# Kernel tuning notes

Measured on AMD Instinct MI355X. Metric: run time of the kernel, lower is better.

Reference implementation:

```python
import jax, jax.numpy as jnp
import numpy as np

HEAD_SIZE = 64
N_EMBED = 1024

def setup_inputs() -> dict:
    key = jax.random.key(0)
    kx, kk, kq, kv = jax.random.split(key, 4)
    x = jax.random.normal(kx, (8, 2048, N_EMBED), dtype=jnp.float32)
    # torch nn.Linear weights: [out_features, in_features]
    s = 1.0 / np.sqrt(N_EMBED)
    Wk = jax.random.uniform(kk, (HEAD_SIZE, N_EMBED), jnp.float32, -s, s)
    Wq = jax.random.uniform(kq, (HEAD_SIZE, N_EMBED), jnp.float32, -s, s)
    Wv = jax.random.uniform(kv, (HEAD_SIZE, N_EMBED), jnp.float32, -s, s)
    return {"x": x, "Wk": Wk, "Wq": Wq, "Wv": Wv}

def reference(x, Wk, Wq, Wv):
    B, T, C = x.shape
    k = x @ Wk.T  # [B,T,H]
    q = x @ Wq.T
    v = x @ Wv.T
    # NOTE: original computes k @ q^T and scales by sqrt(C)=sqrt(n_embed)
    wei = jnp.einsum('btd,bsd->bts', k, q) / jnp.sqrt(jnp.float32(C))
    mask = jnp.tril(jnp.ones((T, T), dtype=bool))
    wei = jnp.where(mask, wei, -jnp.inf)
    wei = jax.nn.softmax(wei, axis=-1)
    return wei @ v  # [B,T,H]
```

## Files before the change

kernel.cpp:

```cpp
#include <hip/hip_runtime.h>
#include <hip/hip_bf16.h>


typedef __attribute__((ext_vector_type(8))) short short8;
typedef __attribute__((ext_vector_type(4))) float f32x4;
typedef __attribute__((ext_vector_type(16))) float f32x16;
typedef unsigned int u32;

#define BATCH 8
#define T 2048
#define CDIM 1024
#define HD 64
#define QK_SCALE 0.04508422f

static __device__ __forceinline__ short f2bf(float f) {
    return __builtin_bit_cast(short, __float2bfloat16(f));
}
static __device__ __forceinline__ float bf2f(unsigned short s) {
    u32 u = ((u32)s) << 16;
    return __builtin_bit_cast(float, u);
}
static __device__ __forceinline__ u32 packbf(float lo, float hi) {
    return (u32)(unsigned short)f2bf(lo) | ((u32)(unsigned short)f2bf(hi) << 16);
}
static __device__ __forceinline__ f32x4 mfma16(short8 a, short8 b, f32x4 c) {
    return __builtin_amdgcn_mfma_f32_16x16x32_bf16(a, b, c, 0, 0, 0);
}
static __device__ __forceinline__ f32x16 mfma32(short8 a, short8 b, f32x16 c) {
    return __builtin_amdgcn_mfma_f32_32x32x16_bf16(a, b, c, 0, 0, 0);
}

__global__ __launch_bounds__(256) void wcvt_kernel(
    const float* __restrict__ Wk, const float* __restrict__ Wq,
    const float* __restrict__ Wv, short* __restrict__ wfrag)
{
    const int t = blockIdx.x * 256 + threadIdx.x;
    const int lane = t & 63, kk = (t >> 6) & 31, d16 = (t >> 11) & 3, p = t >> 13;
    const float* __restrict__ W = (p == 0) ? Wk : (p == 1 ? Wq : Wv);
    const float sc = (p == 0) ? QK_SCALE : 1.0f;
    const float* src = W + (size_t)(d16 * 16 + (lane & 15)) * CDIM
                         + kk * 32 + ((lane >> 4) & 3) * 8;
    f32x4 a = *(const f32x4*)src;
    f32x4 b = *(const f32x4*)(src + 4);
    short8 o;
#pragma unroll
    for (int e = 0; e < 4; ++e) { o[e] = f2bf(a[e] * sc); o[e + 4] = f2bf(b[e] * sc); }
    *(short8*)(wfrag + (size_t)t * 8) = o;
}

#define XLOAD(KC) { \
    xr0 = *(const f32x4*)(xsrc + (KC) * 64); \
    xr1 = *(const f32x4*)(xsrc + (KC) * 64 + 4); }

#define XWRITE(BASE) { \
    short8 v = { f2bf(xr0[0]), f2bf(xr0[1]), f2bf(xr0[2]), f2bf(xr0[3]), \
                 f2bf(xr1[0]), f2bf(xr1[1]), f2bf(xr1[2]), f2bf(xr1[3]) }; \
    *(short8*)((BASE) + srow * 128 + ((sseg * 16) ^ ((srow & 7) << 4))) = v; }

#define BLOAD(DST, KC) \
    _Pragma("unroll") for (int u = 0; u < 6; ++u) \
        DST[u] = *(const short8*)&wfrag[(size_t)((cg * 3 + (u % 3)) * 32 + (KC) * 2 + (u / 3)) * 512 + lane * 8];

#define COMPUTE(XBASE, B) \
    _Pragma("unroll") for (int kkL = 0; kkL < 2; ++kkL) { \
        short8 af0 = *(short8*)((XBASE) + c * 128 + ((kkL * 64 + g * 16) ^ ((c & 7) << 4))); \
        short8 af1 = *(short8*)((XBASE) + (16 + c) * 128 + ((kkL * 64 + g * 16) ^ ((c & 7) << 4))); \
        _Pragma("unroll") for (int j = 0; j < 3; ++j) { \
            acc[0][j] = mfma16(af0, B[kkL * 3 + j], acc[0][j]); \
            acc[1][j] = mfma16(af1, B[kkL * 3 + j], acc[1][j]); } }

__global__ __launch_bounds__(256) void proj_kernel(
    const float* __restrict__ x, const short* __restrict__ wfrag,
    short* __restrict__ kfrag, short* __restrict__ qfrag, short* __restrict__ vfrag)
{
    __shared__ __align__(16) char lds[16384];
    char* X0 = lds;
    char* X1 = lds + 4096;

    const int tid = threadIdx.x, cg = tid >> 6, lane = tid & 63;
    const int c = lane & 15, g = lane >> 4;
    const int srow = tid >> 3, sseg = tid & 7;
    const int row0 = blockIdx.x * 32;
    const float* __restrict__ xsrc = x + (size_t)(row0 + srow) * CDIM + sseg * 8;

    f32x4 acc[2][3] = {};
    short8 bA[6], bB[6];
    f32x4 xr0, xr1;

    XLOAD(0)
    XWRITE(X0)
    BLOAD(bA, 0)
    __syncthreads();

    for (int c2 = 0; c2 < 8; ++c2) {
        const int cB = 2 * c2 + 1;
        BLOAD(bB, cB)
        XLOAD(cB)
        COMPUTE(X0, bA)
        XWRITE(X1)
        __syncthreads();
        if (c2 < 7) {
            BLOAD(bA, cB + 1)
            XLOAD(cB + 1)
        }
        COMPUTE(X1, bB)
        if (c2 < 7) {
            XWRITE(X0)
        }
        __syncthreads();
    }

    short* st_k = (short*)lds;
    short* st_q = (short*)(lds + 4608);
    short* st_v = (short*)(lds + 9216);
#pragma unroll
    for (int j = 0; j < 3; ++j) {
        const int q = cg * 3 + j, p = q >> 2, d16 = q & 3;
#pragma unroll
        for (int rh = 0; rh < 2; ++rh)
#pragma unroll
            for (int r = 0; r < 4; ++r) {
                const int mrow = rh * 16 + g * 4 + r;
                const short v = f2bf(acc[rh][j][r]);
                if (p == 0)      st_k[mrow * 72 + d16 * 16 + c] = v;
                else if (p == 1) st_q[mrow * 72 + d16 * 16 + c] = v;
                else             st_v[(d16 * 16 + c) * 40 + mrow] = v;
            }
    }
    __syncthreads();

    const int b = row0 >> 11, i = (row0 & 2047) >> 5;
    const size_t tb = ((size_t)(b * 64 + i)) * 4;
    const int l5 = lane & 31, h = lane >> 5;
    const int fq = cg;

    short8 kv = *(short8*)&st_k[l5 * 72 + fq * 16 + h * 8];
    *(short8*)&kfrag[(tb + fq) * 512 + lane * 8] = kv;
    short8 qv = *(short8*)&st_q[l5 * 72 + fq * 16 + h * 8];
    *(short8*)&qfrag[(tb + fq) * 512 + lane * 8] = qv;
    const int dh = fq >> 1, ssub = fq & 1;
    short8 vv = *(short8*)&st_v[(dh * 32 + l5) * 40 + ssub * 16 + h * 8];
    *(short8*)&vfrag[(tb + fq) * 512 + lane * 8] = vv;
}

__global__ __launch_bounds__(512) void attn_kernel(
    const short* __restrict__ kfrag, const short* __restrict__ qfrag,
    const short* __restrict__ vfrag, float* __restrict__ out)
{
    const int tid = threadIdx.x, wid = tid >> 6, lane = tid & 63;
    const int l5 = lane & 31, h = lane >> 5;
    const int bx = blockIdx.x;
    const int i = 63 - (bx >> 3);
    const int b = bx & 7;
    const int t0 = i * 32;

    __shared__ u32   sO[8][32][32];
    __shared__ float sML[8][2][32];

    const short* __restrict__ kb = kfrag + ((size_t)(b * 64 + i)) * 2048;
    const short* __restrict__ qb = qfrag + ((size_t)b * 64) * 2048;
    const short* __restrict__ vb = vfrag + ((size_t)b * 64) * 2048;

    short8 kf[4];
#pragma unroll
    for (int ks = 0; ks < 4; ++ks)
        kf[ks] = *(const short8*)&kb[ks * 512 + lane * 8];

    float m = -1e30f, l = 0.f;
    f32x16 o0 = {}, o1 = {};

    short8 qf[4], vf[4], qn[4], vn[4];
#pragma unroll
    for (int ks = 0; ks < 4; ++ks) {
        qf[ks] = *(const short8*)&qb[((size_t)wid * 4 + ks) * 512 + lane * 8];
        vf[ks] = *(const short8*)&vb[((size_t)wid * 4 + ks) * 512 + lane * 8];
    }

    for (int st = wid; st <= i; st += 8) {
        f32x16 Cs = {};
#pragma unroll
        for (int ks = 0; ks < 4; ++ks)
            Cs = mfma32(qf[ks], kf[ks], Cs);

        if (st + 8 <= i) {
#pragma unroll
            for (int ks = 0; ks < 4; ++ks) {
                qn[ks] = *(const short8*)&qb[((size_t)(st + 8) * 4 + ks) * 512 + lane * 8];
                vn[ks] = *(const short8*)&vb[((size_t)(st + 8) * 4 + ks) * 512 + lane * 8];
            }
        }

        if (st == i) {
#pragma unroll
            for (int r = 0; r < 16; ++r) {
                const int srow = (r & 3) + 8 * (r >> 2) + 4 * h;
                if (srow > l5) Cs[r] = -1e30f;
            }
        }
        float mx = fmaxf(Cs[0], Cs[1]);
#pragma unroll
        for (int r = 2; r < 16; ++r) mx = fmaxf(mx, Cs[r]);
        mx = fmaxf(mx, __shfl_xor(mx, 32));
        if (!__all(mx <= m)) {
            const float mnew = fmaxf(m, mx);
            const float alpha = exp2f(m - mnew);
            m = mnew;
            l *= alpha;
#pragma unroll
            for (int r = 0; r < 16; ++r) { o0[r] *= alpha; o1[r] *= alpha; }
        }
        u32 pk[8];
        float rs = 0.f;
#pragma unroll
        for (int q = 0; q < 8; ++q) {
            const float e0 = exp2f(Cs[2 * q] - m);
            const float e1 = exp2f(Cs[2 * q + 1] - m);
            rs += e0 + e1;
            pk[q] = packbf(e0, e1);
        }
        rs += __shfl_xor(rs, 32);
        l += rs;

        u32 w0 = pk[0], w2 = pk[2];
        asm volatile("v_permlane32_swap_b32 %0, %1" : "+v"(w0), "+v"(w2));
        u32 w1 = pk[1], w3 = pk[3];
        asm volatile("v_permlane32_swap_b32 %0, %1" : "+v"(w1), "+v"(w3));
        u32 w4 = pk[4], w6 = pk[6];
        asm volatile("v_permlane32_swap_b32 %0, %1" : "+v"(w4), "+v"(w6));
        u32 w5 = pk[5], w7 = pk[7];
        asm volatile("v_permlane32_swap_b32 %0, %1" : "+v"(w5), "+v"(w7));
        short8 pf0, pf1;
        pf0[0] = (short)(w0 & 0xffff); pf0[1] = (short)(w0 >> 16);
        pf0[2] = (short)(w1 & 0xffff); pf0[3] = (short)(w1 >> 16);
        pf0[4] = (short)(w2 & 0xffff); pf0[5] = (short)(w2 >> 16);
        pf0[6] = (short)(w3 & 0xffff); pf0[7] = (short)(w3 >> 16);
        pf1[0] = (short)(w4 & 0xffff); pf1[1] = (short)(w4 >> 16);
        pf1[2] = (short)(w5 & 0xffff); pf1[3] = (short)(w5 >> 16);
        pf1[4] = (short)(w6 & 0xffff); pf1[5] = (short)(w6 >> 16);
        pf1[6] = (short)(w7 & 0xffff); pf1[7] = (short)(w7 >> 16);

        o0 = mfma32(vf[0], pf0, o0);
        o0 = mfma32(vf[1], pf1, o0);
        o1 = mfma32(vf[2], pf0, o1);
        o1 = mfma32(vf[3], pf1, o1);

#pragma unroll
        for (int ks = 0; ks < 4; ++ks) { qf[ks] = qn[ks]; vf[ks] = vn[ks]; }
    }

#pragma unroll
    for (int q = 0; q < 8; ++q) {
        const int dp = (q & 1) + 4 * (q >> 1) + 2 * h;
        sO[wid][dp][l5]      = packbf(o0[2 * q], o0[2 * q + 1]);
        sO[wid][16 + dp][l5] = packbf(o1[2 * q], o1[2 * q + 1]);
    }
    if (h == 0) { sML[wid][0][l5] = m; sML[wid][1][l5] = l; }
    __syncthreads();

    float M = -1e30f;
#pragma unroll
    for (int p = 0; p < 8; ++p) M = fmaxf(M, sML[p][0][l5]);
    float L = 0.f;
    float av[4] = {};
#pragma unroll
    for (int p = 0; p < 8; ++p) {
        const float w = exp2f(sML[p][0][l5] - M);
        L += w * sML[p][1][l5];
#pragma unroll
        for (int dd2 = 0; dd2 < 2; ++dd2) {
            const u32 v = sO[p][wid * 4 + h * 2 + dd2][l5];
            av[2 * dd2]     += w * bf2f((unsigned short)(v & 0xffff));
            av[2 * dd2 + 1] += w * bf2f((unsigned short)(v >> 16));
        }
    }
    const float inv = 1.f / L;
    f32x4 r = { av[0] * inv, av[1] * inv, av[2] * inv, av[3] * inv };
    *(f32x4*)&out[((size_t)b * T + t0 + l5) * HD + wid * 8 + h * 4] = r;
}

extern "C" void kernel_launch(void* const* d_in, const int* in_sizes, int n_in,
                              void* d_out, int out_size, void* d_ws, size_t ws_size,
                              hipStream_t stream) {
    const float* x  = (const float*)d_in[0];
    const float* Wk = (const float*)d_in[1];
    const float* Wq = (const float*)d_in[2];
    const float* Wv = (const float*)d_in[3];
    float* out = (float*)d_out;

    short* kfrag = (short*)d_ws;
    short* qfrag = kfrag + (size_t)BATCH * T * HD;
    short* vfrag = qfrag + (size_t)BATCH * T * HD;
    short* wfrag = vfrag + (size_t)BATCH * T * HD;

    wcvt_kernel<<<96, 256, 0, stream>>>(Wk, Wq, Wv, wfrag);
    proj_kernel<<<512, 256, 0, stream>>>(x, wfrag, kfrag, qfrag, vfrag);
    attn_kernel<<<512, 512, 0, stream>>>(kfrag, qfrag, vfrag, out);
}
```

Baseline: 43.07 us.

## Split projection output columns across two blocks to double proj grid

The projection kernel now launches 1024 blocks. Each block computes half of the 192 K/Q/V output columns for a 32-row tile: the first half covers K plus part of Q, the second covers the rest of Q plus V. Each wave now holds one 16-row group with three accumulators instead of two row groups, which cuts register pressure and LDS use. The aim is better occupancy and load balance across the GPU's compute units. The cost is that every x tile is loaded and converted twice, doubling x reads from global memory; adjacent block IDs are arranged so the paired blocks run close together and can share the data through cache.

```diff
diff --git a/kernel.cpp b/kernel.cpp
--- a/kernel.cpp
+++ b/kernel.cpp
@@ -59,31 +59,34 @@
 
 #define BLOAD(DST, KC) \
     _Pragma("unroll") for (int u = 0; u < 6; ++u) \
-        DST[u] = *(const short8*)&wfrag[(size_t)((cg * 3 + (u % 3)) * 32 + (KC) * 2 + (u / 3)) * 512 + lane * 8];
+        DST[u] = *(const short8*)&wfrag[(size_t)((nb * 6 + cg2 * 3 + (u % 3)) * 32 + (KC) * 2 + (u / 3)) * 512 + lane * 8];
 
 #define COMPUTE(XBASE, B) \
     _Pragma("unroll") for (int kkL = 0; kkL < 2; ++kkL) { \
-        short8 af0 = *(short8*)((XBASE) + c * 128 + ((kkL * 64 + g * 16) ^ ((c & 7) << 4))); \
-        short8 af1 = *(short8*)((XBASE) + (16 + c) * 128 + ((kkL * 64 + g * 16) ^ ((c & 7) << 4))); \
-        _Pragma("unroll") for (int j = 0; j < 3; ++j) { \
-            acc[0][j] = mfma16(af0, B[kkL * 3 + j], acc[0][j]); \
-            acc[1][j] = mfma16(af1, B[kkL * 3 + j], acc[1][j]); } }
+        const int arow = rg * 16 + c; \
+        short8 af = *(short8*)((XBASE) + arow * 128 + ((kkL * 64 + g * 16) ^ ((arow & 7) << 4))); \
+        _Pragma("unroll") for (int j = 0; j < 3; ++j) \
+            acc[j] = mfma16(af, B[kkL * 3 + j], acc[j]); }
 
 __global__ __launch_bounds__(256) void proj_kernel(
     const float* __restrict__ x, const short* __restrict__ wfrag,
     short* __restrict__ kfrag, short* __restrict__ qfrag, short* __restrict__ vfrag)
 {
-    __shared__ __align__(16) char lds[16384];
+    __shared__ __align__(16) char lds[12288];
     char* X0 = lds;
     char* X1 = lds + 4096;
 
-    const int tid = threadIdx.x, cg = tid >> 6, lane = tid & 63;
+    const int tid = threadIdx.x, wid = tid >> 6, lane = tid & 63;
     const int c = lane & 15, g = lane >> 4;
+    const int l5 = lane & 31, h = lane >> 5;
+    const int bx = blockIdx.x;
+    const int r8 = bx & 7, nb = (bx >> 3) & 1, hi = bx >> 4;
+    const int row0 = (hi * 8 + r8) * 32;
+    const int rg = wid >> 1, cg2 = wid & 1;
     const int srow = tid >> 3, sseg = tid & 7;
-    const int row0 = blockIdx.x * 32;
     const float* __restrict__ xsrc = x + (size_t)(row0 + srow) * CDIM + sseg * 8;
 
-    f32x4 acc[2][3] = {};
+    f32x4 acc[3] = {};
     short8 bA[6], bB[6];
     f32x4 xr0, xr1;
 
@@ -110,37 +113,39 @@
         __syncthreads();
     }
 
-    short* st_k = (short*)lds;
-    short* st_q = (short*)(lds + 4608);
-    short* st_v = (short*)(lds + 9216);
+    short* st_kq = (short*)lds;
+    short* st_v  = (short*)(lds + 6656);
 #pragma unroll
     for (int j = 0; j < 3; ++j) {
-        const int q = cg * 3 + j, p = q >> 2, d16 = q & 3;
-#pragma unroll
-        for (int rh = 0; rh < 2; ++rh)
-#pragma unroll
-            for (int r = 0; r < 4; ++r) {
-                const int mrow = rh * 16 + g * 4 + r;
-                const short v = f2bf(acc[rh][j][r]);
-                if (p == 0)      st_k[mrow * 72 + d16 * 16 + c] = v;
-                else if (p == 1) st_q[mrow * 72 + d16 * 16 + c] = v;
-                else             st_v[(d16 * 16 + c) * 40 + mrow] = v;
-            }
+        const int qq = cg2 * 3 + j;
+#pragma unroll
+        for (int r = 0; r < 4; ++r) {
+            const int mrow = rg * 16 + g * 4 + r;
+            const short v = f2bf(acc[j][r]);
+            if (nb == 0 || qq < 2) st_kq[mrow * 104 + qq * 16 + c] = v;
+            else                   st_v[((qq - 2) * 16 + c) * 40 + mrow] = v;
+        }
     }
     __syncthreads();
 
     const int b = row0 >> 11, i = (row0 & 2047) >> 5;
     const size_t tb = ((size_t)(b * 64 + i)) * 4;
-    const int l5 = lane & 31, h = lane >> 5;
-    const int fq = cg;
-
-    short8 kv = *(short8*)&st_k[l5 * 72 + fq * 16 + h * 8];
-    *(short8*)&kfrag[(tb + fq) * 512 + lane * 8] = kv;
-    short8 qv = *(short8*)&st_q[l5 * 72 + fq * 16 + h * 8];
-    *(short8*)&qfrag[(tb + fq) * 512 + lane * 8] = qv;
-    const int dh = fq >> 1, ssub = fq & 1;
-    short8 vv = *(short8*)&st_v[(dh * 32 + l5) * 40 + ssub * 16 + h * 8];
-    *(short8*)&vfrag[(tb + fq) * 512 + lane * 8] = vv;
+    if (nb == 0) {
+        short8 kv = *(short8*)&st_kq[l5 * 104 + wid * 16 + h * 8];
+        *(short8*)&kfrag[(tb + wid) * 512 + lane * 8] = kv;
+        if (wid < 2) {
+            short8 qv = *(short8*)&st_kq[l5 * 104 + (4 + wid) * 16 + h * 8];
+            *(short8*)&qfrag[(tb + wid) * 512 + lane * 8] = qv;
+        }
+    } else {
+        if (wid < 2) {
+            short8 qv = *(short8*)&st_kq[l5 * 104 + wid * 16 + h * 8];
+            *(short8*)&qfrag[(tb + 2 + wid) * 512 + lane * 8] = qv;
+        }
+        const int dh = wid >> 1, ssub = wid & 1;
+        short8 vv = *(short8*)&st_v[(dh * 32 + l5) * 40 + ssub * 16 + h * 8];
+        *(short8*)&vfrag[(tb + wid) * 512 + lane * 8] = vv;
+    }
 }
 
 __global__ __launch_bounds__(512) void attn_kernel(
@@ -293,6 +298,6 @@
     short* wfrag = vfrag + (size_t)BATCH * T * HD;
 
     wcvt_kernel<<<96, 256, 0, stream>>>(Wk, Wq, Wv, wfrag);
-    proj_kernel<<<512, 256, 0, stream>>>(x, wfrag, kfrag, qfrag, vfrag);
+    proj_kernel<<<1024, 256, 0, stream>>>(x, wfrag, kfrag, qfrag, vfrag);
     attn_kernel<<<512, 512, 0, stream>>>(kfrag, qfrag, vfrag, out);
 }
```

After: 48.16 us. +11.8%, slower.
